# Performance work log

Measured on AMD Instinct MI355X. Metric: run time of the kernel, lower is better.

The kernel has to match this reference:

```python
import jax, jax.numpy as jnp
import numpy as np

B, I, J, P, D = 64, 512, 512, 32, 8
EPS = 1e-5


def _std(t):
    # standardize over last two dims; torch.std uses ddof=1 (unbiased)
    m = t.mean(axis=(-1, -2), keepdims=True)
    s = t.std(axis=(-1, -2), keepdims=True, ddof=1)
    return (t - m) / (s + EPS)


def _flat_softmax(t):
    # softmax over the flattened trailing two dims (torch: flatten(1).softmax(1))
    sh = t.shape
    return jax.nn.softmax(t.reshape(sh[0], sh[1], -1), axis=-1).reshape(sh)


def setup_inputs() -> dict:
    key = jax.random.key(0)
    ks = jax.random.split(key, 10)

    def xav(k, shape):
        # xavier_uniform with relu gain, fan over last two dims
        fan_in, fan_out = shape[-2], shape[-1]
        lim = float(np.sqrt(2.0) * np.sqrt(6.0 / (fan_in + fan_out)))
        return jax.random.uniform(k, shape, jnp.float32, -lim, lim)

    return {
        "x": jax.random.normal(ks[0], (B, I, J), jnp.float32),
        "o_xj": xav(ks[1], (D, J, P)),
        "o_xi": xav(ks[2], (D, I, P)),
        "p_xj": xav(ks[3], (D, I, P)),
        "p_xi": xav(ks[4], (D, J, P)),
        "rel_o_xj": xav(ks[5], (D, J, P)),
        "rel_o_xi": xav(ks[6], (D, I, P)),
        "rel_p_xj": xav(ks[7], (D, P, P)),
        "rel_p_xi": xav(ks[8], (D, P, P)),
        "gamma": jnp.ones((D, 1), jnp.float32),
        "beta": jnp.zeros((D, 1), jnp.float32),
    }


def reference(x, o_xj, o_xi, p_xj, p_xi, rel_o_xj, rel_o_xi, rel_p_xj, rel_p_xi, gamma, beta):
    # Eval-mode reference: dropout is identity. Depth loop vectorized via a leading d axis.
    scale = (I / P) * (J / P)
    x_mean = x.mean(axis=(-1, -2), keepdims=True)[:, None] * scale  # [B,1,1,1]
    x_std = x.std(axis=(-1, -2), keepdims=True, ddof=1)[:, None] * scale

    # relative-mass terms on the original input
    o_rel_xj_sum = _flat_softmax(jnp.einsum('bij,djp->bdip', x, rel_o_xj)).sum(-2)  # [B,D,P]
    o_rel_xi_sum = _flat_softmax(jnp.einsum('bij,dip->bdjp', x, rel_o_xi)).sum(-2)  # [B,D,P]

    # original transforms
    o_t_xj = _std(jnp.tanh(jnp.einsum('bij,djp->bdip', x, o_xj)))   # [B,D,I,P]
    o_t_xi = _std(jnp.tanh(jnp.einsum('bij,dip->bdjp', x, o_xi)))   # [B,D,J,P]

    # permuted transforms -> [B,D,P,P]
    p_t_xj = _std(jnp.tanh(jnp.einsum('bdip,diq->bdpq', o_t_xj, p_xj)))
    p_t_xi = _std(jnp.tanh(jnp.einsum('bdjp,djq->bdqp', o_t_xi, p_xi)))

    # relative-mass terms on the projected tensors
    p_rel_xj_sum = _flat_softmax(jnp.einsum('bdpq,dqr->bdpr', p_t_xj, rel_p_xj)).sum(-2)
    p_rel_xi_sum = _flat_softmax(jnp.einsum('bdpq,dqr->bdpr', p_t_xi, rel_p_xi)).sum(-2)

    fj = jnp.sqrt(o_rel_xj_sum / p_rel_xj_sum)[..., None]  # [B,D,P,1]
    fi = jnp.sqrt(o_rel_xi_sum / p_rel_xi_sum)[..., None]

    xb = jnp.tanh((p_t_xj * fj) * jnp.swapaxes(p_t_xi * fi, -1, -2))
    xb = _std(xb) * x_std + x_mean
    xb = xb * gamma[None, :, :, None] + beta[None, :, :, None]
    return xb.sum(axis=1) / D  # [B,P,P]
```

## Files before the change

### kernel.cpp

```cpp
#include <hip/hip_runtime.h>
#include <math.h>

static constexpr float EPSF = 1e-5f;

typedef short bf16x8 __attribute__((ext_vector_type(8)));
typedef float f32x4 __attribute__((ext_vector_type(4)));
typedef ushort u16x8 __attribute__((ext_vector_type(8)));

__device__ inline ushort bf16rn(float f) {
  unsigned u = __float_as_uint(f);
  unsigned r = (u + 0x7FFFu + ((u >> 16) & 1u)) >> 16;
  return (ushort)r;
}
__device__ inline float bf2f(ushort u) { return __uint_as_float(((unsigned)u) << 16); }
__device__ inline void split2(float f, ushort& hi, ushort& lo) {
  ushort h = bf16rn(f);
  float hf = bf2f(h);
  hi = h;
  lo = bf16rn(f - hf);
}
__device__ inline float fast_tanh(float x) {
  float e = __expf(2.f * x);
  return 1.f - 2.f * __builtin_amdgcn_rcpf(e + 1.f);
}

__device__ inline void gload16(const ushort* g, ushort* l) {
  __builtin_amdgcn_global_load_lds((const __attribute__((address_space(1))) void*)g,
                                   (__attribute__((address_space(3))) void*)l, 16, 0, 0);
}

__device__ inline size_t tiled_addr(int row, int k) {
  return (size_t)(row >> 7) * 65536 + (size_t)(k >> 5) * 4096 +
         (size_t)((k >> 3) & 3) * 1024 + (size_t)(row & 127) * 8 + (k & 7);
}

__global__ __launch_bounds__(256) void conv_pack(
    const float* __restrict__ x,
    const float* __restrict__ o_xj, const float* __restrict__ o_xi,
    const float* __restrict__ rel_o_xj, const float* __restrict__ rel_o_xi,
    const float* __restrict__ p_xj, const float* __restrict__ p_xi,
    ushort* __restrict__ xhi, ushort* __restrict__ xthi,
    ushort* __restrict__ wjhi, ushort* __restrict__ wihi,
    ushort* __restrict__ Wthi, ushort* __restrict__ Wtlo,
    float* __restrict__ colWs,
    float* __restrict__ bpart) {
  const int bx = blockIdx.x;
  const int tid = threadIdx.x;
  if (bx >= 4352) {
    const int pd = bx - 4352;
    const int path = pd >> 3, d = pd & 7;
    const float* src = (path ? p_xi : p_xj) + (size_t)d * 16384;
    ushort* whi = Wthi + (size_t)pd * 16384;
    ushort* wlo = Wtlo + (size_t)pd * 16384;
    __shared__ float buf[64][33];
    float cw = 0.f;
    const int q = tid >> 3, je8 = (tid & 7) * 8;
    for (int j0 = 0; j0 < 512; j0 += 64) {
      for (int l = tid; l < 2048; l += 256) buf[l >> 5][l & 31] = src[(size_t)j0 * 32 + l];
      __syncthreads();
      u16x8 h8, l8;
      #pragma unroll
      for (int e = 0; e < 8; ++e) {
        float fv = buf[je8 + e][q];
        cw += fv;
        ushort h, l; split2(fv, h, l);
        h8[e] = h; l8[e] = l;
      }
      *reinterpret_cast<u16x8*>(&whi[(size_t)q * 512 + j0 + je8]) = h8;
      *reinterpret_cast<u16x8*>(&wlo[(size_t)q * 512 + j0 + je8]) = l8;
      __syncthreads();
    }
    cw += __shfl_xor(cw, 1); cw += __shfl_xor(cw, 2); cw += __shfl_xor(cw, 4);
    if ((tid & 7) == 0) colWs[(size_t)pd * 32 + q] = cw;
    return;
  }
  if (bx >= 4096) {
    int u = (bx - 4096) * 256 + tid;
    int path = u >> 15;
    int v = u & 32767;
    int c = v >> 6;
    int k0 = (v & 63) * 8;
    int d = c >> 6, s = (c >> 5) & 1, p = c & 31;
    const float* src = path ? (s ? rel_o_xi : o_xi) : (s ? rel_o_xj : o_xj);
    u16x8 h8;
    #pragma unroll
    for (int e = 0; e < 8; ++e) h8[e] = bf16rn(src[((size_t)d * 512 + k0 + e) * 32 + p]);
    size_t a = tiled_addr(c, k0);
    ushort* whi = path ? wihi : wjhi;
    *reinterpret_cast<u16x8*>(&whi[a]) = h8;
    return;
  }
  __shared__ float tile[64][65];
  __shared__ float rs[256], rs2[256];
  const int ti = bx & 7, tj = (bx >> 3) & 7, b = bx >> 6;
  const int i0 = ti * 64, j0 = tj * 64;
  const float* xb = x + (size_t)b * 262144;
  const size_t obase = (size_t)b * 262144;
  const int tr = tid >> 4;
  const int tc = (tid & 15) * 4;
  float s = 0.f, s2 = 0.f;
  #pragma unroll
  for (int r = 0; r < 4; ++r) {
    const int row = r * 16 + tr;
    float4 v = *reinterpret_cast<const float4*>(&xb[(size_t)(i0 + row) * 512 + j0 + tc]);
    tile[row][tc + 0] = v.x; tile[row][tc + 1] = v.y;
    tile[row][tc + 2] = v.z; tile[row][tc + 3] = v.w;
    s += v.x + v.y + v.z + v.w;
    s2 += v.x * v.x + v.y * v.y + v.z * v.z + v.w * v.w;
  }
  __syncthreads();
  const int kg = tid >> 5;
  const int rp = tid & 31;
  #pragma unroll
  for (int rr = 0; rr < 2; ++rr) {
    const int li = rp + rr * 32;
    u16x8 h8;
    #pragma unroll
    for (int e = 0; e < 8; ++e) h8[e] = bf16rn(tile[li][kg * 8 + e]);
    *reinterpret_cast<u16x8*>(&xhi[obase + tiled_addr(i0 + li, j0 + kg * 8)]) = h8;
  }
  #pragma unroll
  for (int rr = 0; rr < 2; ++rr) {
    const int lj = rp + rr * 32;
    u16x8 h8;
    #pragma unroll
    for (int e = 0; e < 8; ++e) h8[e] = bf16rn(tile[kg * 8 + e][lj]);
    *reinterpret_cast<u16x8*>(&xthi[obase + tiled_addr(j0 + lj, i0 + kg * 8)]) = h8;
  }
  rs[tid] = s; rs2[tid] = s2;
  __syncthreads();
  for (int off = 128; off > 0; off >>= 1) {
    if (tid < off) { rs[tid] += rs[tid + off]; rs2[tid] += rs2[tid + off]; }
    __syncthreads();
  }
  if (tid == 0) {
    float* pb = bpart + ((size_t)b * 64 + tj * 8 + ti) * 2;
    pb[0] = rs[0]; pb[1] = rs2[0];
  }
}

__global__ __launch_bounds__(256) void mfma_gemm(
    const ushort* __restrict__ xhi, const ushort* __restrict__ xthi,
    const ushort* __restrict__ wjhi, const ushort* __restrict__ wihi,
    ushort* __restrict__ Ttj, ushort* __restrict__ Tti,
    float* __restrict__ pJ, float* __restrict__ pI) {
  const int id = blockIdx.x;
  const int wid = (id & 7) * 256 + (id >> 3);
  const int ct = wid & 3, tm = (wid >> 2) & 3, bz = wid >> 4;
  const int b = bz >> 1, path = bz & 1;
  const ushort* Ahi = (path ? xthi : xhi) + (size_t)b * 262144 + (size_t)tm * 65536;
  const ushort* Bhi = (path ? wihi : wjhi) + (size_t)ct * 65536;
  ushort* Tb = (path ? Tti : Ttj) + (size_t)b * 131072;
  float* partial = path ? pI : pJ;

  __shared__ alignas(16) ushort As_hi[4096], Bs_hi[4096];
  __shared__ float rsum[4], rsq[4], rcol[4][32];

  const int tid = threadIdx.x;
  const int lane = tid & 63, w = tid >> 6;
  const int wr = w >> 1, wc = w & 1;
  const int m0 = tm * 128;

  const int L8 = (w * 64 + lane) * 8;
  const int ldsb0 = (w * 64) * 8;
  const int ldsb1 = 2048 + (w * 64) * 8;

  f32x4 acc[4][4] = {};
  const int fr = lane & 15;
  const int kc = lane >> 4;

  for (int ks = 0; ks < 16; ++ks) {
    const ushort* Ah = Ahi + ks * 4096;
    const ushort* Bh = Bhi + ks * 4096;
    gload16(Ah + L8,        &As_hi[ldsb0]);
    gload16(Ah + 2048 + L8, &As_hi[ldsb1]);
    gload16(Bh + L8,        &Bs_hi[ldsb0]);
    gload16(Bh + 2048 + L8, &Bs_hi[ldsb1]);
    __syncthreads();
    bf16x8 ah[4], bh[4];
    #pragma unroll
    for (int mi = 0; mi < 4; ++mi) {
      const int ra = (kc * 128 + wr * 64 + mi * 16 + fr) * 8;
      ah[mi] = *reinterpret_cast<const bf16x8*>(&As_hi[ra]);
    }
    #pragma unroll
    for (int ni = 0; ni < 4; ++ni) {
      const int rb = (kc * 128 + wc * 64 + ni * 16 + fr) * 8;
      bh[ni] = *reinterpret_cast<const bf16x8*>(&Bs_hi[rb]);
    }
    #pragma unroll
    for (int mi = 0; mi < 4; ++mi)
      #pragma unroll
      for (int ni = 0; ni < 4; ++ni)
        acc[mi][ni] = __builtin_amdgcn_mfma_f32_16x16x32_bf16(ah[mi], bh[ni], acc[mi][ni], 0, 0, 0);
    __syncthreads();
  }

  float lsum = 0.f, lsq = 0.f, cs0 = 0.f, cs1 = 0.f;
  const int d = ct * 2 + wc;
  #pragma unroll
  for (int mi = 0; mi < 4; ++mi) {
    const int rbase = m0 + wr * 64 + mi * 16 + ((lane >> 4) << 2);
    #pragma unroll
    for (int ni = 0; ni < 4; ++ni) {
      if (ni < 2) {
        const int p = ni * 16 + fr;
        float t0 = fast_tanh(acc[mi][ni][0]);
        float t1 = fast_tanh(acc[mi][ni][1]);
        float t2 = fast_tanh(acc[mi][ni][2]);
        float t3 = fast_tanh(acc[mi][ni][3]);
        lsum += t0 + t1 + t2 + t3;
        lsq += t0 * t0 + t1 * t1 + t2 * t2 + t3 * t3;
        ushort4 pk;
        pk.x = bf16rn(t0); pk.y = bf16rn(t1); pk.z = bf16rn(t2); pk.w = bf16rn(t3);
        *reinterpret_cast<ushort4*>(&Tb[((size_t)d * 32 + p) * 512 + rbase]) = pk;
      } else {
        #pragma unroll
        for (int r = 0; r < 4; ++r) {
          float e = __expf(acc[mi][ni][r]);
          if (ni == 2) cs0 += e; else cs1 += e;
        }
      }
    }
  }
  #pragma unroll
  for (int m = 1; m < 64; m <<= 1) { lsum += __shfl_xor(lsum, m); lsq += __shfl_xor(lsq, m); }
  cs0 += __shfl_xor(cs0, 16); cs0 += __shfl_xor(cs0, 32);
  cs1 += __shfl_xor(cs1, 16); cs1 += __shfl_xor(cs1, 32);
  if (lane == 0) { rsum[w] = lsum; rsq[w] = lsq; }
  if (lane < 16) { rcol[w][lane] = cs0; rcol[w][16 + lane] = cs1; }
  __syncthreads();
  if (tid < 64) {
    const int wc2 = tid >> 5, p = tid & 31;
    float* pb = partial + (((size_t)b * 4 + tm) * 8 + ct * 2 + wc2) * 34;
    pb[2 + p] = rcol[wc2][p] + rcol[wc2 + 2][p];
    if (p == 0) {
      pb[0] = rsum[wc2] + rsum[wc2 + 2];
      pb[1] = rsq[wc2] + rsq[wc2 + 2];
    }
  }
}

__global__ __launch_bounds__(256) void stage3_fused(
    const ushort* __restrict__ Ttj, const ushort* __restrict__ Tti,
    const ushort* __restrict__ Wthi, const ushort* __restrict__ Wtlo,
    const float* __restrict__ colWs,
    const float* __restrict__ rel_pj, const float* __restrict__ rel_pi,
    const float* __restrict__ pJ, const float* __restrict__ pI,
    const float* __restrict__ bpart,
    const float* __restrict__ gamma_p, const float* __restrict__ beta_p,
    float* __restrict__ xball) {
  const int bd = blockIdx.x;
  const int b = bd >> 3, d = bd & 7;
  const int tid = threadIdx.x;
  const int lane = tid & 63, w = tid >> 6;
  const int path = w >> 1, mt = w & 1;
  const int fr = lane & 15, kg = lane >> 4;

  __shared__ float Vl[2][32][33];
  __shared__ float Rl[2][32][32];
  __shared__ float cred[2][32][33];
  __shared__ float colw_s[64];
  __shared__ float stS[2][34];
  __shared__ float ms[2][2];
  __shared__ float orelT[2];
  __shared__ float pred[4][2];
  __shared__ float csum[2][32];
  __shared__ float stot[2];
  __shared__ float fsc[2][32];
  __shared__ float red[256], red2[256];
  __shared__ float sred[2], sbst[2];

  for (int l = tid; l < 2048; l += 256) {
    const int pp = l >> 10, idx = l & 1023;
    const float* Rsrc = pp ? rel_pi : rel_pj;
    Rl[pp][idx >> 5][idx & 31] = Rsrc[(size_t)d * 1024 + idx];
  }
  if (tid < 64) colw_s[tid] = colWs[(((size_t)(tid >> 5) * 8 + d)) * 32 + (tid & 31)];
  if (tid >= 64 && tid < 132) {
    const int u = tid - 64;
    const int pp = u >= 34, t = pp ? u - 34 : u;
    const float* P = pp ? pI : pJ;
    float v = 0.f;
    #pragma unroll
    for (int tm2 = 0; tm2 < 4; ++tm2) v += P[(((size_t)b * 4 + tm2) * 8 + d) * 34 + t];
    stS[pp][t] = v;
  }
  if (tid >= 192) {
    const int t = tid - 192;
    float s = bpart[(size_t)b * 128 + t * 2];
    float s2 = bpart[(size_t)b * 128 + t * 2 + 1];
    #pragma unroll
    for (int m = 1; m < 64; m <<= 1) { s += __shfl_xor(s, m); s2 += __shfl_xor(s2, m); }
    if (t == 0) {
      const float N = 262144.f;
      float mean = s / N;
      float var = (s2 - s * s / N) / (N - 1.f);
      sbst[0] = mean * 256.f;
      sbst[1] = sqrtf(fmaxf(var, 0.f)) * 256.f;
    }
  }
  __syncthreads();
  if (tid < 2) {
    const float* S = stS[tid];
    const float N = 16384.f;
    float mean = S[0] / N;
    float var = (S[1] - S[0] * S[0] / N) / (N - 1.f);
    ms[tid][0] = mean;
    ms[tid][1] = 1.f / (sqrtf(fmaxf(var, 0.f)) + EPSF);
    float tot = 0.f;
    for (int k = 0; k < 32; ++k) tot += S[2 + k];
    orelT[tid] = tot;
  }

  f32x4 acc0 = {}, acc1 = {};
  const ushort* Whi_p = Wthi + ((size_t)path * 8 + d) * 16384;
  const ushort* Wlo_p = Wtlo + ((size_t)path * 8 + d) * 16384;
  const ushort* Tp = (path ? Tti : Ttj) + ((size_t)b * 8 + d) * 16384;

  if (path == 0) {
    const ushort* Arow = Tp + (size_t)(mt * 16 + fr) * 512;
    const ushort* B0h = Whi_p + (size_t)fr * 512;
    const ushort* B0l = Wlo_p + (size_t)fr * 512;
    const ushort* B1h = Whi_p + (size_t)(16 + fr) * 512;
    const ushort* B1l = Wlo_p + (size_t)(16 + fr) * 512;
    for (int k0 = 0; k0 < 512; k0 += 32) {
      const int ko = k0 + kg * 8;
      bf16x8 a   = *reinterpret_cast<const bf16x8*>(Arow + ko);
      bf16x8 b0h = *reinterpret_cast<const bf16x8*>(B0h + ko);
      bf16x8 b0l = *reinterpret_cast<const bf16x8*>(B0l + ko);
      bf16x8 b1h = *reinterpret_cast<const bf16x8*>(B1h + ko);
      bf16x8 b1l = *reinterpret_cast<const bf16x8*>(B1l + ko);
      acc0 = __builtin_amdgcn_mfma_f32_16x16x32_bf16(a, b0h, acc0, 0, 0, 0);
      acc0 = __builtin_amdgcn_mfma_f32_16x16x32_bf16(a, b0l, acc0, 0, 0, 0);
      acc1 = __builtin_amdgcn_mfma_f32_16x16x32_bf16(a, b1h, acc1, 0, 0, 0);
      acc1 = __builtin_amdgcn_mfma_f32_16x16x32_bf16(a, b1l, acc1, 0, 0, 0);
    }
  } else {
    const ushort* Ahr = Whi_p + (size_t)(mt * 16 + fr) * 512;
    const ushort* Alr = Wlo_p + (size_t)(mt * 16 + fr) * 512;
    const ushort* B0 = Tp + (size_t)fr * 512;
    const ushort* B1 = Tp + (size_t)(16 + fr) * 512;
    for (int k0 = 0; k0 < 512; k0 += 32) {
      const int ko = k0 + kg * 8;
      bf16x8 ah = *reinterpret_cast<const bf16x8*>(Ahr + ko);
      bf16x8 al = *reinterpret_cast<const bf16x8*>(Alr + ko);
      bf16x8 b0 = *reinterpret_cast<const bf16x8*>(B0 + ko);
      bf16x8 b1 = *reinterpret_cast<const bf16x8*>(B1 + ko);
      acc0 = __builtin_amdgcn_mfma_f32_16x16x32_bf16(ah, b0, acc0, 0, 0, 0);
      acc0 = __builtin_amdgcn_mfma_f32_16x16x32_bf16(al, b0, acc0, 0, 0, 0);
      acc1 = __builtin_amdgcn_mfma_f32_16x16x32_bf16(ah, b1, acc1, 0, 0, 0);
      acc1 = __builtin_amdgcn_mfma_f32_16x16x32_bf16(al, b1, acc1, 0, 0, 0);
    }
  }
  __syncthreads();

  const float mean = ms[path][0], rstd = ms[path][1];
  float tv0[4], tv1[4];
  float ls = 0.f, lq = 0.f;
  #pragma unroll
  for (int r = 0; r < 4; ++r) {
    const int rowm = mt * 16 + kg * 4 + r;
    {
      const float cw = (path == 0) ? colw_s[fr] : colw_s[32 + rowm];
      float t = fast_tanh((acc0[r] - mean * cw) * rstd);
      tv0[r] = t; ls += t; lq += t * t;
    }
    {
      const float cw = (path == 0) ? colw_s[16 + fr] : colw_s[32 + rowm];
      float t = fast_tanh((acc1[r] - mean * cw) * rstd);
      tv1[r] = t; ls += t; lq += t * t;
    }
  }
  #pragma unroll
  for (int m = 1; m < 64; m <<= 1) { ls += __shfl_xor(ls, m); lq += __shfl_xor(lq, m); }
  if (lane == 0) { pred[w][0] = ls; pred[w][1] = lq; }
  __syncthreads();
  {
    const float S = pred[path * 2][0] + pred[path * 2 + 1][0];
    const float SS = pred[path * 2][1] + pred[path * 2 + 1][1];
    const float m2 = S / 1024.f;
    const float var = (SS - S * S / 1024.f) / 1023.f;
    const float r2 = 1.f / (sqrtf(fmaxf(var, 0.f)) + EPSF);
    #pragma unroll
    for (int r = 0; r < 4; ++r) {
      const int rowm = mt * 16 + kg * 4 + r;
      Vl[path][rowm][fr] = (tv0[r] - m2) * r2;
      Vl[path][rowm][16 + fr] = (tv1[r] - m2) * r2;
    }
  }
  __syncthreads();

  {
    const int t2 = tid & 127;
    const int prow = t2 >> 2, c8 = (t2 & 3) * 8;
    float racc[8] = {};
    #pragma unroll
    for (int c = 0; c < 32; ++c) {
      const float v = Vl[path][prow][c];
      #pragma unroll
      for (int e = 0; e < 8; ++e) racc[e] = fmaf(v, Rl[path][c][c8 + e], racc[e]);
    }
    #pragma unroll
    for (int e = 0; e < 8; ++e) cred[path][prow][c8 + e] = __expf(racc[e]);
  }
  __syncthreads();
  if (tid < 64) {
    const int pp = tid >> 5, q = tid & 31;
    float s = 0.f;
    #pragma unroll 8
    for (int p = 0; p < 32; ++p) s += cred[pp][p][q];
    csum[pp][q] = s;
  }
  __syncthreads();
  if (tid < 2) {
    float tot = 0.f;
    for (int k = 0; k < 32; ++k) tot += csum[tid][k];
    stot[tid] = tot;
  }
  __syncthreads();
  if (tid < 64) {
    const int pp = tid >> 5, q = tid & 31;
    fsc[pp][q] = sqrtf((stS[pp][2 + q] / orelT[pp]) * stot[pp] / csum[pp][q]);
  }
  __syncthreads();

  const int row = tid >> 3, c4 = (tid & 7) * 4;
  float xv[4]; float ls2 = 0.f, lq2 = 0.f;
  #pragma unroll
  for (int e = 0; e < 4; ++e) {
    const int q = c4 + e;
    float v = fast_tanh(Vl[0][row][q] * fsc[0][row] * Vl[1][q][row] * fsc[1][q]);
    xv[e] = v; ls2 += v; lq2 += v * v;
  }
  red[tid] = ls2; red2[tid] = lq2;
  __syncthreads();
  for (int off = 128; off > 0; off >>= 1) {
    if (tid < off) { red[tid] += red[tid + off]; red2[tid] += red2[tid + off]; }
    __syncthreads();
  }
  if (tid == 0) {
    float s = red[0], ss = red2[0];
    float m = s / 1024.f;
    float var = (ss - s * s / 1024.f) / 1023.f;
    sred[0] = m; sred[1] = 1.f / (sqrtf(fmaxf(var, 0.f)) + EPSF);
  }
  __syncthreads();
  const float m3 = sred[0], r3 = sred[1];
  const float xm = sbst[0], xs = sbst[1];
  const float g = gamma_p[d], be = beta_p[d];
  #pragma unroll
  for (int e = 0; e < 4; ++e) {
    float v = (xv[e] - m3) * r3 * xs + xm;
    xball[(size_t)bd * 1024 + row * 32 + c4 + e] = v * g + be;
  }
}

__global__ void final_kernel(const float* __restrict__ xball, float* __restrict__ out) {
  const int b = blockIdx.x;
  for (int e = threadIdx.x; e < 1024; e += 256) {
    float s = 0.f;
    #pragma unroll
    for (int d = 0; d < 8; ++d) s += xball[((size_t)(b * 8 + d)) * 1024 + e];
    out[(size_t)b * 1024 + e] = s * 0.125f;
  }
}

extern "C" void kernel_launch(void* const* d_in, const int* in_sizes, int n_in,
                              void* d_out, int out_size, void* d_ws, size_t ws_size,
                              hipStream_t stream) {
  const float* x        = (const float*)d_in[0];
  const float* o_xj     = (const float*)d_in[1];
  const float* o_xi     = (const float*)d_in[2];
  const float* p_xj     = (const float*)d_in[3];
  const float* p_xi     = (const float*)d_in[4];
  const float* rel_o_xj = (const float*)d_in[5];
  const float* rel_o_xi = (const float*)d_in[6];
  const float* rel_p_xj = (const float*)d_in[7];
  const float* rel_p_xi = (const float*)d_in[8];
  const float* gamma_p  = (const float*)d_in[9];
  const float* beta_p   = (const float*)d_in[10];
  float* out = (float*)d_out;

  char* base = (char*)d_ws;
  ushort* xhi  = (ushort*)base; base += (size_t)33554432;
  ushort* xthi = (ushort*)base; base += (size_t)33554432;
  ushort* wjhi = (ushort*)base; base += 524288;
  ushort* wihi = (ushort*)base; base += 524288;
  ushort* Ttj  = (ushort*)base; base += (size_t)16777216;
  ushort* Tti  = (ushort*)base; base += (size_t)16777216;
  ushort* Wthi = (ushort*)base; base += 524288;
  ushort* Wtlo = (ushort*)base; base += 524288;
  float* colWs = (float*)base;  base += 2048;
  float* pJ    = (float*)base;  base += 278528;
  float* pI    = (float*)base;  base += 278528;
  float* bpart = (float*)base;  base += 32768;
  float* xball = (float*)base;  base += 2097152;

  hipLaunchKernelGGL(conv_pack, dim3(4368), dim3(256), 0, stream,
                     x, o_xj, o_xi, rel_o_xj, rel_o_xi, p_xj, p_xi,
                     xhi, xthi, wjhi, wihi, Wthi, Wtlo, colWs, bpart);
  hipLaunchKernelGGL(mfma_gemm, dim3(2048), dim3(256), 0, stream,
                     xhi, xthi, wjhi, wihi, Ttj, Tti, pJ, pI);
  hipLaunchKernelGGL(stage3_fused, dim3(512), dim3(256), 0, stream,
                     Ttj, Tti, Wthi, Wtlo, colWs, rel_p_xj, rel_p_xi, pJ, pI, bpart,
                     gamma_p, beta_p, xball);
  hipLaunchKernelGGL(final_kernel, dim3(64), dim3(256), 0, stream, xball, out);
}
```

Baseline: 106.0 us.

## Widen GEMM block tile to 256 output columns to halve A-tile reloads

Each mfma_gemm block now computes a 128x256 output tile (four depth slices) instead of 128x128, which halves the grid to 1024 blocks. Each A (x) tile is loaded once per two former blocks, cutting global and LDS traffic for the large x operand. The epilogue is reworked to produce per-depth statistics for two depths per wave. In exchange, accumulator registers double (128 floats per lane), which may lower occupancy, and the smaller grid gives fewer blocks per CU.

```diff
diff --git a/kernel.cpp b/kernel.cpp
--- a/kernel.cpp
+++ b/kernel.cpp
@@ -145,16 +145,16 @@
     ushort* __restrict__ Ttj, ushort* __restrict__ Tti,
     float* __restrict__ pJ, float* __restrict__ pI) {
   const int id = blockIdx.x;
-  const int wid = (id & 7) * 256 + (id >> 3);
-  const int ct = wid & 3, tm = (wid >> 2) & 3, bz = wid >> 4;
+  const int wid = (id & 7) * 128 + (id >> 3);
+  const int ct = wid & 1, tm = (wid >> 1) & 3, bz = wid >> 3;
   const int b = bz >> 1, path = bz & 1;
   const ushort* Ahi = (path ? xthi : xhi) + (size_t)b * 262144 + (size_t)tm * 65536;
-  const ushort* Bhi = (path ? wihi : wjhi) + (size_t)ct * 65536;
+  const ushort* Bbase = (path ? wihi : wjhi) + (size_t)ct * 131072;
   ushort* Tb = (path ? Tti : Ttj) + (size_t)b * 131072;
   float* partial = path ? pI : pJ;
 
-  __shared__ alignas(16) ushort As_hi[4096], Bs_hi[4096];
-  __shared__ float rsum[4], rsq[4], rcol[4][32];
+  __shared__ alignas(16) ushort As_hi[4096], Bs_hi[8192];
+  __shared__ float rsum[4][2], rsq[4][2], rcol[4][2][32];
 
   const int tid = threadIdx.x;
   const int lane = tid & 63, w = tid >> 6;
@@ -162,81 +162,88 @@
   const int m0 = tm * 128;
 
   const int L8 = (w * 64 + lane) * 8;
-  const int ldsb0 = (w * 64) * 8;
-  const int ldsb1 = 2048 + (w * 64) * 8;
-
-  f32x4 acc[4][4] = {};
+  const int ldsA0 = w * 512;
+  const int ldsA1 = 2048 + w * 512;
+
+  f32x4 acc[4][8] = {};
   const int fr = lane & 15;
   const int kc = lane >> 4;
 
   for (int ks = 0; ks < 16; ++ks) {
     const ushort* Ah = Ahi + ks * 4096;
-    const ushort* Bh = Bhi + ks * 4096;
-    gload16(Ah + L8,        &As_hi[ldsb0]);
-    gload16(Ah + 2048 + L8, &As_hi[ldsb1]);
-    gload16(Bh + L8,        &Bs_hi[ldsb0]);
-    gload16(Bh + 2048 + L8, &Bs_hi[ldsb1]);
+    const ushort* Bh = Bbase + ks * 4096;
+    gload16(Ah + L8,                &As_hi[ldsA0]);
+    gload16(Ah + 2048 + L8,         &As_hi[ldsA1]);
+    gload16(Bh + L8,                &Bs_hi[ldsA0]);
+    gload16(Bh + 2048 + L8,         &Bs_hi[ldsA1]);
+    gload16(Bh + 65536 + L8,        &Bs_hi[4096 + ldsA0]);
+    gload16(Bh + 65536 + 2048 + L8, &Bs_hi[4096 + ldsA1]);
     __syncthreads();
-    bf16x8 ah[4], bh[4];
+    bf16x8 ah[4];
     #pragma unroll
     for (int mi = 0; mi < 4; ++mi) {
       const int ra = (kc * 128 + wr * 64 + mi * 16 + fr) * 8;
       ah[mi] = *reinterpret_cast<const bf16x8*>(&As_hi[ra]);
     }
     #pragma unroll
-    for (int ni = 0; ni < 4; ++ni) {
-      const int rb = (kc * 128 + wc * 64 + ni * 16 + fr) * 8;
-      bh[ni] = *reinterpret_cast<const bf16x8*>(&Bs_hi[rb]);
-    }
-    #pragma unroll
-    for (int mi = 0; mi < 4; ++mi)
+    for (int ni = 0; ni < 8; ++ni) {
+      const int rb = wc * 4096 + (kc * 128 + ni * 16 + fr) * 8;
+      bf16x8 bf = *reinterpret_cast<const bf16x8*>(&Bs_hi[rb]);
       #pragma unroll
-      for (int ni = 0; ni < 4; ++ni)
-        acc[mi][ni] = __builtin_amdgcn_mfma_f32_16x16x32_bf16(ah[mi], bh[ni], acc[mi][ni], 0, 0, 0);
+      for (int mi = 0; mi < 4; ++mi)
+        acc[mi][ni] = __builtin_amdgcn_mfma_f32_16x16x32_bf16(ah[mi], bf, acc[mi][ni], 0, 0, 0);
+    }
     __syncthreads();
   }
 
-  float lsum = 0.f, lsq = 0.f, cs0 = 0.f, cs1 = 0.f;
-  const int d = ct * 2 + wc;
+  float lsum[2] = {0.f, 0.f}, lsq[2] = {0.f, 0.f};
+  float cs[2][2] = {};
   #pragma unroll
   for (int mi = 0; mi < 4; ++mi) {
     const int rbase = m0 + wr * 64 + mi * 16 + ((lane >> 4) << 2);
     #pragma unroll
-    for (int ni = 0; ni < 4; ++ni) {
-      if (ni < 2) {
-        const int p = ni * 16 + fr;
+    for (int ni = 0; ni < 8; ++ni) {
+      const int dd = ni >> 2;
+      const int s = (ni >> 1) & 1;
+      if (s == 0) {
+        const int p = (ni & 1) * 16 + fr;
+        const int d = ct * 4 + wc * 2 + dd;
         float t0 = fast_tanh(acc[mi][ni][0]);
         float t1 = fast_tanh(acc[mi][ni][1]);
         float t2 = fast_tanh(acc[mi][ni][2]);
         float t3 = fast_tanh(acc[mi][ni][3]);
-        lsum += t0 + t1 + t2 + t3;
-        lsq += t0 * t0 + t1 * t1 + t2 * t2 + t3 * t3;
+        lsum[dd] += t0 + t1 + t2 + t3;
+        lsq[dd] += t0 * t0 + t1 * t1 + t2 * t2 + t3 * t3;
         ushort4 pk;
         pk.x = bf16rn(t0); pk.y = bf16rn(t1); pk.z = bf16rn(t2); pk.w = bf16rn(t3);
         *reinterpret_cast<ushort4*>(&Tb[((size_t)d * 32 + p) * 512 + rbase]) = pk;
       } else {
-        #pragma unroll
-        for (int r = 0; r < 4; ++r) {
-          float e = __expf(acc[mi][ni][r]);
-          if (ni == 2) cs0 += e; else cs1 += e;
-        }
+        float e0 = __expf(acc[mi][ni][0]);
+        float e1 = __expf(acc[mi][ni][1]);
+        float e2 = __expf(acc[mi][ni][2]);
+        float e3 = __expf(acc[mi][ni][3]);
+        cs[dd][ni & 1] += e0 + e1 + e2 + e3;
       }
     }
   }
   #pragma unroll
-  for (int m = 1; m < 64; m <<= 1) { lsum += __shfl_xor(lsum, m); lsq += __shfl_xor(lsq, m); }
-  cs0 += __shfl_xor(cs0, 16); cs0 += __shfl_xor(cs0, 32);
-  cs1 += __shfl_xor(cs1, 16); cs1 += __shfl_xor(cs1, 32);
-  if (lane == 0) { rsum[w] = lsum; rsq[w] = lsq; }
-  if (lane < 16) { rcol[w][lane] = cs0; rcol[w][16 + lane] = cs1; }
-  __syncthreads();
-  if (tid < 64) {
-    const int wc2 = tid >> 5, p = tid & 31;
-    float* pb = partial + (((size_t)b * 4 + tm) * 8 + ct * 2 + wc2) * 34;
-    pb[2 + p] = rcol[wc2][p] + rcol[wc2 + 2][p];
+  for (int dd = 0; dd < 2; ++dd) {
+    #pragma unroll
+    for (int m = 1; m < 64; m <<= 1) { lsum[dd] += __shfl_xor(lsum[dd], m); lsq[dd] += __shfl_xor(lsq[dd], m); }
+    cs[dd][0] += __shfl_xor(cs[dd][0], 16); cs[dd][0] += __shfl_xor(cs[dd][0], 32);
+    cs[dd][1] += __shfl_xor(cs[dd][1], 16); cs[dd][1] += __shfl_xor(cs[dd][1], 32);
+    if (lane == 0) { rsum[w][dd] = lsum[dd]; rsq[w][dd] = lsq[dd]; }
+    if (lane < 16) { rcol[w][dd][lane] = cs[dd][0]; rcol[w][dd][16 + lane] = cs[dd][1]; }
+  }
+  __syncthreads();
+  if (tid < 128) {
+    const int dl = tid >> 5, p = tid & 31;
+    const int wc2 = dl >> 1, dd = dl & 1;
+    float* pb = partial + (((size_t)b * 4 + tm) * 8 + ct * 4 + dl) * 34;
+    pb[2 + p] = rcol[wc2][dd][p] + rcol[2 + wc2][dd][p];
     if (p == 0) {
-      pb[0] = rsum[wc2] + rsum[wc2 + 2];
-      pb[1] = rsq[wc2] + rsq[wc2 + 2];
+      pb[0] = rsum[wc2][dd] + rsum[2 + wc2][dd];
+      pb[1] = rsq[wc2][dd] + rsq[2 + wc2][dd];
     }
   }
 }
@@ -500,7 +507,7 @@
   hipLaunchKernelGGL(conv_pack, dim3(4368), dim3(256), 0, stream,
                      x, o_xj, o_xi, rel_o_xj, rel_o_xi, p_xj, p_xi,
                      xhi, xthi, wjhi, wihi, Wthi, Wtlo, colWs, bpart);
-  hipLaunchKernelGGL(mfma_gemm, dim3(2048), dim3(256), 0, stream,
+  hipLaunchKernelGGL(mfma_gemm, dim3(1024), dim3(256), 0, stream,
                      xhi, xthi, wjhi, wihi, Ttj, Tti, pJ, pI);
   hipLaunchKernelGGL(stage3_fused, dim3(512), dim3(256), 0, stream,
                      Ttj, Tti, Wthi, Wtlo, colWs, rel_p_xj, rel_p_xi, pJ, pI, bpart,
```

Result: slower. 136.6 us (+28.9%).
